# Kernel tuning notes

Hardware: AMD Instinct MI355X
Metric: run time of the kernel (lower is better)

## Reference

```python
import jax, jax.numpy as jnp
import numpy as np

THR = 0.2        # config['thr']
BORDER_RM = 2    # config['border_rm']


def _border_valid(h, w, b):
    # Flattened [h*w] bool mask: True for cells at least b away from every border.
    r = jnp.arange(h)
    c = jnp.arange(w)
    vr = (r >= b) & (r < h - b)
    vc = (c >= b) & (c < w - b)
    return (vr[:, None] & vc[None, :]).reshape(-1)


def setup_inputs() -> dict:
    key = jax.random.key(0)
    h0c, w0c, h1c, w1c = 60, 80, 60, 80   # coarse grid (640x480 / 8)
    N = 4
    conf = jax.random.uniform(key, (N, h0c * w0c, h1c * w1c), dtype=jnp.float32)
    return {"conf_matrix": conf, "h0c": h0c, "w0c": w0c, "h1c": h1c, "w1c": w1c}


def reference(conf_matrix, h0c, w0c, h1c, w1c):
    # conf_matrix: [N, L, S], L = h0c*w0c, S = h1c*w1c
    valid0 = _border_valid(h0c, w0c, BORDER_RM)   # [L]
    valid1 = _border_valid(h1c, w1c, BORDER_RM)   # [S]

    # threshold + border removal (equivalent to mask_border on the 5D view)
    mask = (conf_matrix > THR) & valid0[None, :, None] & valid1[None, None, :]

    # mutual nearest neighbor: keep only entries that are both row-max and col-max
    rowmax = jnp.max(conf_matrix, axis=2, keepdims=True)   # [N, L, 1]
    colmax = jnp.max(conf_matrix, axis=1, keepdims=True)   # [N, 1, S]
    mask = mask & (conf_matrix == rowmax) & (conf_matrix == colmax)

    # torch's mask.max(dim=2) on bool -> (any, first-True index)
    all_j_ids = jnp.argmax(mask, axis=2)                   # [N, L] int
    mask_v = jnp.any(mask, axis=2)                         # [N, L] bool
    mconf = jnp.take_along_axis(conf_matrix, all_j_ids[:, :, None], axis=2)[:, :, 0]
    mconf = mconf * mask_v                                 # zero where no match
    return mconf, mask_v, all_j_ids
```

## Files before the change

### kernel.cpp

```cpp
#include <hip/hip_runtime.h>
#include <cfloat>

#define THRV 0.2f
#define H0 60
#define W0 80
#define H1 60
#define W1 80
#define LL (H0 * W0)
#define SS (H1 * W1)
#define BR 2
#define KCAND 8
#define RPB 12

__global__ void __launch_bounds__(256) fused_scan(
    const float* __restrict__ conf,
    unsigned int* __restrict__ colmax,
    float* __restrict__ rowmaxArr,
    int* __restrict__ candCnt,
    int* __restrict__ candPos)
{
  const int tid = threadIdx.x;
  const int n = blockIdx.y;
  const int l0 = blockIdx.x * RPB;

  __shared__ float wred[4];
  __shared__ int lcnt;
  __shared__ int lpos[KCAND];
  if (tid == 0) lcnt = 0;

  float4 cm[5];
#pragma unroll
  for (int k = 0; k < 5; ++k) cm[k] = make_float4(0.f, 0.f, 0.f, 0.f);
  __syncthreads();

  for (int r = 0; r < RPB; ++r) {
    const int l = l0 + r;
    const float4* rowp = (const float4*)(conf + ((size_t)n * LL + l) * SS);

    float4 d[5];
    float tm = -1.f;
#pragma unroll
    for (int k = 0; k < 5; ++k) {
      const int i = tid + 256 * k;
      if (i < 1200) {
        float4 v = rowp[i];
        d[k] = v;
        cm[k].x = fmaxf(cm[k].x, v.x);
        cm[k].y = fmaxf(cm[k].y, v.y);
        cm[k].z = fmaxf(cm[k].z, v.z);
        cm[k].w = fmaxf(cm[k].w, v.w);
        tm = fmaxf(tm, fmaxf(fmaxf(v.x, v.y), fmaxf(v.z, v.w)));
      } else {
        d[k] = make_float4(-1.f, -1.f, -1.f, -1.f);
      }
    }

#pragma unroll
    for (int off = 32; off; off >>= 1) tm = fmaxf(tm, __shfl_xor(tm, off, 64));
    if ((tid & 63) == 0) wred[tid >> 6] = tm;
    __syncthreads();
    const float rowmax = fmaxf(fmaxf(wred[0], wred[1]), fmaxf(wred[2], wred[3]));

    const int r0 = l / W0, c0 = l % W0;
    const bool valid0 = (r0 >= BR) && (r0 < H0 - BR) && (c0 >= BR) && (c0 < W0 - BR);

    if (valid0 && rowmax > THRV) {
#pragma unroll
      for (int k = 0; k < 5; ++k) {
        const int i = tid + 256 * k;
        const float4 v = d[k];
        if (v.x == rowmax) { int ix = atomicAdd(&lcnt, 1); if (ix < KCAND) lpos[ix] = 4 * i + 0; }
        if (v.y == rowmax) { int ix = atomicAdd(&lcnt, 1); if (ix < KCAND) lpos[ix] = 4 * i + 1; }
        if (v.z == rowmax) { int ix = atomicAdd(&lcnt, 1); if (ix < KCAND) lpos[ix] = 4 * i + 2; }
        if (v.w == rowmax) { int ix = atomicAdd(&lcnt, 1); if (ix < KCAND) lpos[ix] = 4 * i + 3; }
      }
    }
    __syncthreads();

    const int row = n * LL + l;
    const int c = lcnt;
    if (tid == 0) { candCnt[row] = c; rowmaxArr[row] = rowmax; }
    if (tid < (c < KCAND ? c : KCAND)) candPos[row * KCAND + tid] = lpos[tid];
    __syncthreads();
    if (tid == 0) lcnt = 0;
  }

#pragma unroll
  for (int k = 0; k < 5; ++k) {
    const int i = tid + 256 * k;
    if (i < 1200) {
      unsigned int* base = colmax + n * SS + 4 * i;
      atomicMax(base + 0, __float_as_uint(cm[k].x));
      atomicMax(base + 1, __float_as_uint(cm[k].y));
      atomicMax(base + 2, __float_as_uint(cm[k].z));
      atomicMax(base + 3, __float_as_uint(cm[k].w));
    }
  }
}

__global__ void __launch_bounds__(256) resolve(
    const float* __restrict__ conf,
    const unsigned int* __restrict__ colmax,
    const float* __restrict__ rowmaxArr,
    const int* __restrict__ candCnt,
    const int* __restrict__ candPos,
    float* __restrict__ out, int N)
{
  const int row = blockIdx.x * 256 + threadIdx.x;
  const int NL = N * LL;
  if (row >= NL) return;
  const int n = row / LL;

  float mconf = 0.f, mv = 0.f, jid = 0.f;
  const int c = candCnt[row];
  if (c > 0) {
    const float rowmax = rowmaxArr[row];
    const unsigned int rmu = __float_as_uint(rowmax);
    const unsigned int* cmn = colmax + n * SS;
    int best = 0x7fffffff;
    if (c <= KCAND) {
      for (int i = 0; i < c; ++i) {
        const int s = candPos[row * KCAND + i];
        const int r1 = s / W1, c1 = s % W1;
        const bool valid1 = (r1 >= BR) && (r1 < H1 - BR) && (c1 >= BR) && (c1 < W1 - BR);
        if (valid1 && cmn[s] == rmu && s < best) best = s;
      }
    } else {
      const float* rp = conf + (size_t)row * SS;
      for (int s = 0; s < SS; ++s) {
        if (rp[s] == rowmax) {
          const int r1 = s / W1, c1 = s % W1;
          const bool valid1 = (r1 >= BR) && (r1 < H1 - BR) && (c1 >= BR) && (c1 < W1 - BR);
          if (valid1 && cmn[s] == rmu) { best = s; break; }
        }
      }
    }
    if (best != 0x7fffffff) { mconf = rowmax; mv = 1.f; jid = (float)best; }
  }
  out[row] = mconf;
  out[NL + row] = mv;
  out[2 * NL + row] = jid;
}

extern "C" void kernel_launch(void* const* d_in, const int* in_sizes, int n_in,
                              void* d_out, int out_size, void* d_ws, size_t ws_size,
                              hipStream_t stream) {
  const float* conf = (const float*)d_in[0];
  const int N = in_sizes[0] / (LL * SS);
  float* out = (float*)d_out;

  unsigned int* colmax = (unsigned int*)d_ws;
  float* rowmaxArr = (float*)(colmax + (size_t)N * SS);
  int* candCnt = (int*)(rowmaxArr + (size_t)N * LL);
  int* candPos = candCnt + (size_t)N * LL;

  hipMemsetAsync(colmax, 0, (size_t)N * SS * sizeof(unsigned int), stream);

  dim3 g1(LL / RPB, N);
  fused_scan<<<g1, 256, 0, stream>>>(conf, colmax, rowmaxArr, candCnt, candPos);

  const int NL = N * LL;
  resolve<<<(NL + 255) / 256, 256, 0, stream>>>(conf, colmax, rowmaxArr, candCnt, candPos, out, N);
}
```

Baseline: 594.5 us.

## Scan rows per wavefront and replace column atomics with two-stage reduction

```diff
diff --git a/kernel.cpp b/kernel.cpp
--- a/kernel.cpp
+++ b/kernel.cpp
@@ -1,5 +1,4 @@
 #include <hip/hip_runtime.h>
-#include <cfloat>
 
 #define THRV 0.2f
 #define H0 60
@@ -10,102 +9,139 @@
 #define SS (H1 * W1)
 #define BR 2
 #define KCAND 8
-#define RPB 12
-
-__global__ void __launch_bounds__(256) fused_scan(
+#define RPW 16
+#define WPN (LL / RPW)
+#define NQ4 (SS / 4)
+#define KMAX 19
+
+__global__ void __launch_bounds__(256) scan_kernel(
     const float* __restrict__ conf,
-    unsigned int* __restrict__ colmax,
+    float* __restrict__ colPart,
     float* __restrict__ rowmaxArr,
     int* __restrict__ candCnt,
     int* __restrict__ candPos)
 {
-  const int tid = threadIdx.x;
+  const int lane = threadIdx.x & 63;
+  const int wid = threadIdx.x >> 6;
   const int n = blockIdx.y;
-  const int l0 = blockIdx.x * RPB;
-
-  __shared__ float wred[4];
-  __shared__ int lcnt;
-  __shared__ int lpos[KCAND];
-  if (tid == 0) lcnt = 0;
-
-  float4 cm[5];
-#pragma unroll
-  for (int k = 0; k < 5; ++k) cm[k] = make_float4(0.f, 0.f, 0.f, 0.f);
-  __syncthreads();
-
-  for (int r = 0; r < RPB; ++r) {
+  const int w = blockIdx.x * 4 + wid;
+  const int l0 = w * RPW;
+
+  float4 cm[KMAX];
+#pragma unroll
+  for (int k = 0; k < KMAX; ++k) cm[k] = make_float4(0.f, 0.f, 0.f, 0.f);
+
+  for (int r = 0; r < RPW; ++r) {
     const int l = l0 + r;
-    const float4* rowp = (const float4*)(conf + ((size_t)n * LL + l) * SS);
-
-    float4 d[5];
-    float tm = -1.f;
-#pragma unroll
-    for (int k = 0; k < 5; ++k) {
-      const int i = tid + 256 * k;
-      if (i < 1200) {
-        float4 v = rowp[i];
-        d[k] = v;
+    const float4* __restrict__ rowp =
+        (const float4*)(conf + ((size_t)n * LL + l) * SS);
+
+    float4 d[KMAX];
+#pragma unroll
+    for (int k = 0; k < KMAX; ++k) {
+      const int q = lane + 64 * k;
+      if (q < NQ4) d[k] = rowp[q];
+    }
+
+    float lmA = -1.f, lmB = -1.f;
+    int fiA = 0, fiB = 0, cnA = 0, cnB = 0;
+#define UPD(LM, FI, CN, V, S)                          \
+  {                                                    \
+    const float _v = (V);                              \
+    const bool _gt = _v > LM;                          \
+    const bool _eq = _v == LM;                         \
+    CN = _gt ? 1 : (CN + (_eq ? 1 : 0));               \
+    FI = _gt ? (S) : FI;                               \
+    LM = _gt ? _v : LM;                                \
+  }
+#pragma unroll
+    for (int k = 0; k < KMAX; ++k) {
+      const int q = lane + 64 * k;
+      if (q < NQ4) {
+        const float4 v = d[k];
         cm[k].x = fmaxf(cm[k].x, v.x);
         cm[k].y = fmaxf(cm[k].y, v.y);
         cm[k].z = fmaxf(cm[k].z, v.z);
         cm[k].w = fmaxf(cm[k].w, v.w);
-        tm = fmaxf(tm, fmaxf(fmaxf(v.x, v.y), fmaxf(v.z, v.w)));
-      } else {
-        d[k] = make_float4(-1.f, -1.f, -1.f, -1.f);
-      }
-    }
-
-#pragma unroll
-    for (int off = 32; off; off >>= 1) tm = fmaxf(tm, __shfl_xor(tm, off, 64));
-    if ((tid & 63) == 0) wred[tid >> 6] = tm;
-    __syncthreads();
-    const float rowmax = fmaxf(fmaxf(wred[0], wred[1]), fmaxf(wred[2], wred[3]));
+        const int s0 = 4 * q;
+        if (k & 1) {
+          UPD(lmB, fiB, cnB, v.x, s0 + 0);
+          UPD(lmB, fiB, cnB, v.y, s0 + 1);
+          UPD(lmB, fiB, cnB, v.z, s0 + 2);
+          UPD(lmB, fiB, cnB, v.w, s0 + 3);
+        } else {
+          UPD(lmA, fiA, cnA, v.x, s0 + 0);
+          UPD(lmA, fiA, cnA, v.y, s0 + 1);
+          UPD(lmA, fiA, cnA, v.z, s0 + 2);
+          UPD(lmA, fiA, cnA, v.w, s0 + 3);
+        }
+      }
+    }
+#undef UPD
+    float lm;
+    int fidx, cnt;
+    if (lmA > lmB) {
+      lm = lmA; fidx = fiA; cnt = cnA;
+    } else if (lmB > lmA) {
+      lm = lmB; fidx = fiB; cnt = cnB;
+    } else {
+      lm = lmA; fidx = min(fiA, fiB); cnt = cnA + cnB;
+    }
+
+    float rowmax = lm;
+#pragma unroll
+    for (int off = 32; off; off >>= 1)
+      rowmax = fmaxf(rowmax, __shfl_xor(rowmax, off, 64));
 
     const int r0 = l / W0, c0 = l % W0;
-    const bool valid0 = (r0 >= BR) && (r0 < H0 - BR) && (c0 >= BR) && (c0 < W0 - BR);
-
+    const bool valid0 =
+        (r0 >= BR) && (r0 < H0 - BR) && (c0 >= BR) && (c0 < W0 - BR);
+
+    const bool isc = (lm == rowmax);
+    const unsigned long long m = __ballot(isc);
+    const unsigned long long mMulti = __ballot(isc && cnt > 1);
+    const int row = n * LL + l;
     if (valid0 && rowmax > THRV) {
-#pragma unroll
-      for (int k = 0; k < 5; ++k) {
-        const int i = tid + 256 * k;
-        const float4 v = d[k];
-        if (v.x == rowmax) { int ix = atomicAdd(&lcnt, 1); if (ix < KCAND) lpos[ix] = 4 * i + 0; }
-        if (v.y == rowmax) { int ix = atomicAdd(&lcnt, 1); if (ix < KCAND) lpos[ix] = 4 * i + 1; }
-        if (v.z == rowmax) { int ix = atomicAdd(&lcnt, 1); if (ix < KCAND) lpos[ix] = 4 * i + 2; }
-        if (v.w == rowmax) { int ix = atomicAdd(&lcnt, 1); if (ix < KCAND) lpos[ix] = 4 * i + 3; }
-      }
-    }
-    __syncthreads();
-
-    const int row = n * LL + l;
-    const int c = lcnt;
-    if (tid == 0) { candCnt[row] = c; rowmaxArr[row] = rowmax; }
-    if (tid < (c < KCAND ? c : KCAND)) candPos[row * KCAND + tid] = lpos[tid];
-    __syncthreads();
-    if (tid == 0) lcnt = 0;
-  }
-
-#pragma unroll
-  for (int k = 0; k < 5; ++k) {
-    const int i = tid + 256 * k;
-    if (i < 1200) {
-      unsigned int* base = colmax + n * SS + 4 * i;
-      atomicMax(base + 0, __float_as_uint(cm[k].x));
-      atomicMax(base + 1, __float_as_uint(cm[k].y));
-      atomicMax(base + 2, __float_as_uint(cm[k].z));
-      atomicMax(base + 3, __float_as_uint(cm[k].w));
-    }
-  }
-}
-
-__global__ void __launch_bounds__(256) resolve(
-    const float* __restrict__ conf,
-    const unsigned int* __restrict__ colmax,
-    const float* __restrict__ rowmaxArr,
-    const int* __restrict__ candCnt,
-    const int* __restrict__ candPos,
-    float* __restrict__ out, int N)
-{
+      const int slot = __popcll(m & ((1ull << lane) - 1ull));
+      if (isc && slot < KCAND) candPos[row * KCAND + slot] = fidx;
+      if (lane == 0) {
+        candCnt[row] = mMulti ? 0x7fffffff : (int)__popcll(m);
+        rowmaxArr[row] = rowmax;
+      }
+    } else if (lane == 0) {
+      candCnt[row] = 0;
+      rowmaxArr[row] = rowmax;
+    }
+  }
+
+  float4* __restrict__ pp = (float4*)(colPart + ((size_t)n * WPN + w) * SS);
+#pragma unroll
+  for (int k = 0; k < KMAX; ++k) {
+    const int q = lane + 64 * k;
+    if (q < NQ4) pp[q] = cm[k];
+  }
+}
+
+__global__ void __launch_bounds__(256) colreduce_kernel(
+    const float* __restrict__ colPart, float* __restrict__ colmax, int N) {
+  const int t = blockIdx.x * 256 + threadIdx.x;
+  if (t >= N * SS) return;
+  const int n = t / SS, s = t % SS;
+  const float* __restrict__ p = colPart + (size_t)n * WPN * SS + s;
+  float m0 = 0.f, m1 = 0.f, m2 = 0.f, m3 = 0.f;
+  for (int w = 0; w < WPN; w += 4) {
+    m0 = fmaxf(m0, p[(size_t)w * SS]);
+    m1 = fmaxf(m1, p[(size_t)(w + 1) * SS]);
+    m2 = fmaxf(m2, p[(size_t)(w + 2) * SS]);
+    m3 = fmaxf(m3, p[(size_t)(w + 3) * SS]);
+  }
+  colmax[t] = fmaxf(fmaxf(m0, m1), fmaxf(m2, m3));
+}
+
+__global__ void __launch_bounds__(256) resolve_kernel(
+    const float* __restrict__ conf, const float* __restrict__ colmax,
+    const float* __restrict__ rowmaxArr, const int* __restrict__ candCnt,
+    const int* __restrict__ candPos, float* __restrict__ out, int N) {
   const int row = blockIdx.x * 256 + threadIdx.x;
   const int NL = N * LL;
   if (row >= NL) return;
@@ -115,23 +151,24 @@
   const int c = candCnt[row];
   if (c > 0) {
     const float rowmax = rowmaxArr[row];
-    const unsigned int rmu = __float_as_uint(rowmax);
-    const unsigned int* cmn = colmax + n * SS;
+    const float* __restrict__ cmn = colmax + n * SS;
     int best = 0x7fffffff;
     if (c <= KCAND) {
       for (int i = 0; i < c; ++i) {
         const int s = candPos[row * KCAND + i];
         const int r1 = s / W1, c1 = s % W1;
-        const bool valid1 = (r1 >= BR) && (r1 < H1 - BR) && (c1 >= BR) && (c1 < W1 - BR);
-        if (valid1 && cmn[s] == rmu && s < best) best = s;
+        const bool valid1 =
+            (r1 >= BR) && (r1 < H1 - BR) && (c1 >= BR) && (c1 < W1 - BR);
+        if (valid1 && cmn[s] == rowmax && s < best) best = s;
       }
     } else {
-      const float* rp = conf + (size_t)row * SS;
+      const float* __restrict__ rp = conf + (size_t)row * SS;
       for (int s = 0; s < SS; ++s) {
         if (rp[s] == rowmax) {
           const int r1 = s / W1, c1 = s % W1;
-          const bool valid1 = (r1 >= BR) && (r1 < H1 - BR) && (c1 >= BR) && (c1 < W1 - BR);
-          if (valid1 && cmn[s] == rmu) { best = s; break; }
+          const bool valid1 =
+              (r1 >= BR) && (r1 < H1 - BR) && (c1 >= BR) && (c1 < W1 - BR);
+          if (valid1 && cmn[s] == rowmax) { best = s; break; }
         }
       }
     }
@@ -149,16 +186,19 @@
   const int N = in_sizes[0] / (LL * SS);
   float* out = (float*)d_out;
 
-  unsigned int* colmax = (unsigned int*)d_ws;
-  float* rowmaxArr = (float*)(colmax + (size_t)N * SS);
+  float* colPart = (float*)d_ws;
+  float* colmax = colPart + (size_t)N * WPN * SS;
+  float* rowmaxArr = colmax + (size_t)N * SS;
   int* candCnt = (int*)(rowmaxArr + (size_t)N * LL);
   int* candPos = candCnt + (size_t)N * LL;
 
-  hipMemsetAsync(colmax, 0, (size_t)N * SS * sizeof(unsigned int), stream);
-
-  dim3 g1(LL / RPB, N);
-  fused_scan<<<g1, 256, 0, stream>>>(conf, colmax, rowmaxArr, candCnt, candPos);
+  dim3 g1(WPN / 4, N);
+  scan_kernel<<<g1, 256, 0, stream>>>(conf, colPart, rowmaxArr, candCnt, candPos);
+
+  const int NS = N * SS;
+  colreduce_kernel<<<(NS + 255) / 256, 256, 0, stream>>>(colPart, colmax, N);
 
   const int NL = N * LL;
-  resolve<<<(NL + 255) / 256, 256, 0, stream>>>(conf, colmax, rowmaxArr, candCnt, candPos, out, N);
-}
+  resolve_kernel<<<(NL + 255) / 256, 256, 0, stream>>>(conf, colmax, rowmaxArr,
+                                                       candCnt, candPos, out, N);
+}
```

Result: faster. 522.8 us (-12.1%).
